# Kernel tuning notes

Measured on AMD Instinct MI355X. Metric: run time of the kernel, lower is better.

The kernel has to match this reference:

```python
import jax, jax.numpy as jnp
import numpy as np

N = 50000
E = 600000
IN_DIM, FEAT_DIM, HID_DIM, OUT_DIM = 256, 128, 128, 64


def _glorot(key, shape):
    fan_in, fan_out = shape[0], shape[1]
    lim = jnp.sqrt(6.0 / (fan_in + fan_out))
    return jax.random.uniform(key, shape, jnp.float32, -lim, lim)


def setup_inputs() -> dict:
    key = jax.random.key(0)
    ks = jax.random.split(key, 10)
    x = jax.random.normal(ks[0], (N, IN_DIM), jnp.float32)
    edge_index = jax.random.randint(ks[1], (2, E), 0, N, jnp.int64)
    return {
        "x": x,
        "edge_index": edge_index,
        # linear_pre: input_dim -> feature_dim
        "W_pre": _glorot(ks[2], (IN_DIM, FEAT_DIM)),
        "b_pre": jnp.zeros((FEAT_DIM,), jnp.float32),
        # conv_first (SAGEConv feature_dim -> hidden_dim): lin_l (neighbors, bias), lin_r (root, no bias)
        "Wl1": _glorot(ks[3], (FEAT_DIM, HID_DIM)),
        "bl1": jnp.zeros((HID_DIM,), jnp.float32),
        "Wr1": _glorot(ks[4], (FEAT_DIM, HID_DIM)),
        # conv_out (SAGEConv hidden_dim -> output_dim)
        "Wl2": _glorot(ks[5], (HID_DIM, OUT_DIM)),
        "bl2": jnp.zeros((OUT_DIM,), jnp.float32),
        "Wr2": _glorot(ks[6], (HID_DIM, OUT_DIM)),
    }


def _sage_conv(x, src, dst, deg_inv, Wl, bl, Wr):
    # mean aggregation of source features at destination nodes
    msgs = x[src]                                            # [E, d]
    aggr = jax.ops.segment_sum(msgs, dst, num_segments=N)    # [N, d]
    aggr = aggr * deg_inv[:, None]
    return aggr @ Wl + bl + x @ Wr


def reference(x, edge_index, W_pre, b_pre, Wl1, bl1, Wr1, Wl2, bl2, Wr2):
    src, dst = edge_index[0], edge_index[1]
    deg = jax.ops.segment_sum(jnp.ones((E,), jnp.float32), dst, num_segments=N)
    deg_inv = jnp.where(deg > 0, 1.0 / jnp.maximum(deg, 1.0), 0.0)

    h = x @ W_pre + b_pre                                    # linear_pre
    h = _sage_conv(h, src, dst, deg_inv, Wl1, bl1, Wr1)      # conv_first
    h = jax.nn.relu(h)
    # dropout: identity in eval mode
    h = _sage_conv(h, src, dst, deg_inv, Wl2, bl2, Wr2)      # conv_out
    norm = jnp.linalg.norm(h, axis=-1, keepdims=True)
    return h / jnp.maximum(norm, 1e-12)                      # F.normalize p=2
```

## Files before the change

### kernel.cpp

```cpp
#include <hip/hip_runtime.h>


#define NN   50000
#define EE   600000
#define NBLK 49
#define NRG  1563
#define GEMM_BLOCKS 512

typedef __attribute__((ext_vector_type(8))) _Float16 h8v;
typedef __attribute__((ext_vector_type(4))) _Float16 h4v;
typedef __attribute__((ext_vector_type(2))) _Float16 h2v;
typedef __attribute__((ext_vector_type(8))) short short8v;
typedef __attribute__((ext_vector_type(4))) float f32x4;

__device__ inline h8v h8zero() {
    return __builtin_bit_cast(h8v, (short8v){0,0,0,0,0,0,0,0});
}

__device__ inline h8v cvt8(const float* __restrict__ p) {
    float4 f0 = *(const float4*)p;
    float4 f1 = *(const float4*)(p + 4);
    h8v a;
    a[0] = (_Float16)f0.x; a[1] = (_Float16)f0.y;
    a[2] = (_Float16)f0.z; a[3] = (_Float16)f0.w;
    a[4] = (_Float16)f1.x; a[5] = (_Float16)f1.y;
    a[6] = (_Float16)f1.z; a[7] = (_Float16)f1.w;
    return a;
}


__global__ __launch_bounds__(256) void k_count(const int* __restrict__ ei,
                                               int* __restrict__ counts) {
    int e = blockIdx.x * 256 + threadIdx.x;
    if (e < EE) atomicAdd(&counts[ei[EE + e]], 1);
}

__global__ __launch_bounds__(256) void k_scan_a(const int* __restrict__ counts,
                                                int* __restrict__ bsums) {
    int b = blockIdx.x, t = threadIdx.x;
    int idx = b * 1024 + t * 4;
    int s = 0;
#pragma unroll
    for (int j = 0; j < 4; ++j)
        if (idx + j < NN) s += counts[idx + j];
#pragma unroll
    for (int off = 32; off > 0; off >>= 1) s += __shfl_down(s, off);
    __shared__ int ls[4];
    if ((t & 63) == 0) ls[t >> 6] = s;
    __syncthreads();
    if (t == 0) bsums[b] = ls[0] + ls[1] + ls[2] + ls[3];
}

__global__ void k_scan_b(int* __restrict__ bsums) {
    int t = threadIdx.x;
    int v = (t < NBLK) ? bsums[t] : 0;
    int orig = v;
#pragma unroll
    for (int off = 1; off < 64; off <<= 1) {
        int u = __shfl_up(v, off);
        if (t >= off) v += u;
    }
    if (t < NBLK) bsums[t] = v - orig;
}

__global__ __launch_bounds__(256) void k_scan_c(const int* __restrict__ counts,
                                                const int* __restrict__ bsums,
                                                int* __restrict__ rowp) {
    int b = blockIdx.x, t = threadIdx.x;
    int lane = t & 63, wave = t >> 6;
    int idx = b * 1024 + t * 4;
    int c[4], s = 0;
#pragma unroll
    for (int j = 0; j < 4; ++j) {
        c[j] = (idx + j < NN) ? counts[idx + j] : 0;
        s += c[j];
    }
    int sv = s;
#pragma unroll
    for (int off = 1; off < 64; off <<= 1) {
        int u = __shfl_up(sv, off);
        if (lane >= off) sv += u;
    }
    __shared__ int lsum[4];
    if (lane == 63) lsum[wave] = sv;
    __syncthreads();
    int woff = 0;
    for (int wv = 0; wv < wave; ++wv) woff += lsum[wv];
    int base = bsums[b] + woff + (sv - s);
#pragma unroll
    for (int j = 0; j < 4; ++j) {
        if (idx + j < NN) { rowp[idx + j] = base; base += c[j]; }
    }
}

__global__ __launch_bounds__(256) void k_scatter(const int* __restrict__ ei,
                                                 const int* __restrict__ rowp,
                                                 int* __restrict__ cursor,
                                                 int* __restrict__ col) {
    int e = blockIdx.x * 256 + threadIdx.x;
    if (e < EE) {
        int d = ei[EE + e];
        int p = atomicAdd(&cursor[d], 1);
        col[rowp[d] + p] = ei[e];
    }
}


__global__ __launch_bounds__(256) void k_fuse(const float* __restrict__ Wpre,
                                              const float* __restrict__ bpre,
                                              const float* __restrict__ Wl1,
                                              const float* __restrict__ Wr1,
                                              _Float16* __restrict__ WAH,
                                              _Float16* __restrict__ WAL,
                                              _Float16* __restrict__ WBH,
                                              _Float16* __restrict__ WBL,
                                              float* __restrict__ bA,
                                              float* __restrict__ bB) {
    int idx = blockIdx.x * 256 + threadIdx.x;
    int which = idx / (257 * 128);
    int rem = idx - which * 257 * 128;
    int i = rem >> 7, j = rem & 127;
    const float* W = which ? Wr1 : Wl1;
    float s = 0.f;
    if (i < 256) {
#pragma unroll 4
        for (int k = 0; k < 128; ++k) s += Wpre[i * 128 + k] * W[k * 128 + j];
        _Float16 h = (_Float16)s;
        _Float16 l = (_Float16)(s - (float)h);
        if (which) { WBH[j * 256 + i] = h; WBL[j * 256 + i] = l; }
        else       { WAH[j * 256 + i] = h; WAL[j * 256 + i] = l; }
    } else {
#pragma unroll 4
        for (int k = 0; k < 128; ++k) s += bpre[k] * W[k * 128 + j];
        if (which) bB[j] = s; else bA[j] = s;
    }
}


__global__ __launch_bounds__(256) void k_pack2(const float* __restrict__ Wl2,
                                               const float* __restrict__ Wr2,
                                               _Float16* __restrict__ W2lH,
                                               _Float16* __restrict__ W2lL,
                                               _Float16* __restrict__ W2rH,
                                               _Float16* __restrict__ W2rL) {
    int idx = blockIdx.x * 256 + threadIdx.x;
    int which = idx >> 13;
    int rem = idx & 8191;
    int k = rem >> 6, m = rem & 63;
    float w = (which ? Wr2 : Wl2)[rem];
    _Float16 h = (_Float16)w;
    _Float16 l = (_Float16)(w - (float)h);
    if (which) { W2rH[m * 128 + k] = h; W2rL[m * 128 + k] = l; }
    else       { W2lH[m * 128 + k] = h; W2lL[m * 128 + k] = l; }
}


__global__ __launch_bounds__(256, 2) void k_gemm_fused(
        const float* __restrict__ x,
        const _Float16* __restrict__ WAH, const _Float16* __restrict__ WAL,
        const _Float16* __restrict__ WBH, const _Float16* __restrict__ WBL,
        const float* __restrict__ bA, const float* __restrict__ bB,
        _Float16* __restrict__ t1, _Float16* __restrict__ r1) {
    const int wave = threadIdx.x >> 6, lane = threadIdx.x & 63;
    const int r = lane & 15, kb = lane >> 4;
    const int gw = blockIdx.x * 4 + wave;
    const int col = ((gw & 7) << 4) + r;

    h8v wah[8], wal[8], wbh[8], wbl[8];
#pragma unroll
    for (int k = 0; k < 8; ++k) {
        size_t off = (size_t)col * 256 + k * 32 + kb * 8;
        wah[k] = *(const h8v*)&WAH[off];
        wal[k] = *(const h8v*)&WAL[off];
        wbh[k] = *(const h8v*)&WBH[off];
        wbl[k] = *(const h8v*)&WBL[off];
    }
    const float biasA = bA[col], biasB = bB[col];

    for (int rg = gw >> 3; rg < NRG; rg += (GEMM_BLOCKS * 4) / 8) {
        const int row0 = rg << 5;
        f32x4 accT[2], accR[2];
#pragma unroll
        for (int a = 0; a < 2; ++a) {
            accT[a] = (f32x4){0.f, 0.f, 0.f, 0.f};
            accR[a] = (f32x4){0.f, 0.f, 0.f, 0.f};
        }
#pragma unroll
        for (int k = 0; k < 8; ++k) {
#pragma unroll
            for (int rt = 0; rt < 2; ++rt) {
                int rr = row0 + rt * 16;
                h8v a = (rr < NN)
                    ? cvt8(&x[(size_t)(rr + r) * 256 + k * 32 + kb * 8])
                    : h8zero();
                accT[rt] = __builtin_amdgcn_mfma_f32_16x16x32_f16(a, wah[k], accT[rt], 0, 0, 0);
                accT[rt] = __builtin_amdgcn_mfma_f32_16x16x32_f16(a, wal[k], accT[rt], 0, 0, 0);
                accR[rt] = __builtin_amdgcn_mfma_f32_16x16x32_f16(a, wbh[k], accR[rt], 0, 0, 0);
                accR[rt] = __builtin_amdgcn_mfma_f32_16x16x32_f16(a, wbl[k], accR[rt], 0, 0, 0);
            }
        }
#pragma unroll
        for (int rt = 0; rt < 2; ++rt) {
            if (row0 + rt * 16 >= NN) continue;
            int rbase = row0 + rt * 16 + kb * 4;
#pragma unroll
            for (int j = 0; j < 4; ++j) {
                t1[(size_t)(rbase + j) * 128 + col] = (_Float16)(accT[rt][j] + biasA);
                r1[(size_t)(rbase + j) * 128 + col] = (_Float16)(accR[rt][j] + biasB);
            }
        }
    }
}


template <int M>
__global__ __launch_bounds__(256, 2) void k_gemm_dual(
        const _Float16* __restrict__ A,
        const _Float16* __restrict__ W1H, const _Float16* __restrict__ W1L,
        const _Float16* __restrict__ W2H, const _Float16* __restrict__ W2L,
        _Float16* __restrict__ T, _Float16* __restrict__ R) {
    constexpr int CS = M / 32;
    const int wave = threadIdx.x >> 6, lane = threadIdx.x & 63;
    const int r = lane & 15, kb = lane >> 4;
    const int gw = blockIdx.x * 4 + wave;
    const int col0 = (gw % CS) << 5;

    h8v b1h[2][4], b1l[2][4], b2h[2][4], b2l[2][4];
#pragma unroll
    for (int nt = 0; nt < 2; ++nt)
#pragma unroll
        for (int k = 0; k < 4; ++k) {
            size_t off = (size_t)(col0 + nt * 16 + r) * 128 + k * 32 + kb * 8;
            b1h[nt][k] = *(const h8v*)&W1H[off];
            b1l[nt][k] = *(const h8v*)&W1L[off];
            b2h[nt][k] = *(const h8v*)&W2H[off];
            b2l[nt][k] = *(const h8v*)&W2L[off];
        }

    const int stride = (GEMM_BLOCKS * 4) / CS;
    for (int rg = gw / CS; rg < NRG; rg += stride) {
        const int row0 = rg << 5;
        f32x4 accT[2][2], accR[2][2];
#pragma unroll
        for (int a = 0; a < 2; ++a)
#pragma unroll
            for (int b = 0; b < 2; ++b) {
                accT[a][b] = (f32x4){0.f, 0.f, 0.f, 0.f};
                accR[a][b] = (f32x4){0.f, 0.f, 0.f, 0.f};
            }
#pragma unroll
        for (int k = 0; k < 4; ++k) {
            h8v ah[2];
#pragma unroll
            for (int rt = 0; rt < 2; ++rt) {
                int rr = row0 + rt * 16;
                ah[rt] = (rr < NN) ? *(const h8v*)&A[(size_t)(rr + r) * 128 + k * 32 + kb * 8]
                                   : h8zero();
            }
#pragma unroll
            for (int rt = 0; rt < 2; ++rt)
#pragma unroll
                for (int nt = 0; nt < 2; ++nt) {
                    accT[rt][nt] = __builtin_amdgcn_mfma_f32_16x16x32_f16(ah[rt], b1h[nt][k], accT[rt][nt], 0, 0, 0);
                    accT[rt][nt] = __builtin_amdgcn_mfma_f32_16x16x32_f16(ah[rt], b1l[nt][k], accT[rt][nt], 0, 0, 0);
                    accR[rt][nt] = __builtin_amdgcn_mfma_f32_16x16x32_f16(ah[rt], b2h[nt][k], accR[rt][nt], 0, 0, 0);
                    accR[rt][nt] = __builtin_amdgcn_mfma_f32_16x16x32_f16(ah[rt], b2l[nt][k], accR[rt][nt], 0, 0, 0);
                }
        }
#pragma unroll
        for (int rt = 0; rt < 2; ++rt) {
            if (row0 + rt * 16 >= NN) continue;
            int rbase = row0 + rt * 16 + kb * 4;
#pragma unroll
            for (int nt = 0; nt < 2; ++nt) {
                int c = col0 + nt * 16 + r;
#pragma unroll
                for (int j = 0; j < 4; ++j) {
                    T[(size_t)(rbase + j) * M + c] = (_Float16)accT[rt][nt][j];
                    R[(size_t)(rbase + j) * M + c] = (_Float16)accR[rt][nt][j];
                }
            }
        }
    }
}


__global__ __launch_bounds__(256) void k_aggr1(const _Float16* __restrict__ t1,
                                               const _Float16* __restrict__ r1,
                                               const int* __restrict__ rowp,
                                               const int* __restrict__ counts,
                                               const int* __restrict__ col,
                                               const float* __restrict__ bl1,
                                               _Float16* __restrict__ h1) {
    int node = blockIdx.x * 4 + (threadIdx.x >> 6);
    int lane = threadIdx.x & 63;
    if (node >= NN) return;
    int half = lane >> 5, sl = lane & 31;
    int e0 = rowp[node], cnt = counts[node];
    float a0 = 0.f, a1 = 0.f, a2 = 0.f, a3 = 0.f;
    const h4v* T = (const h4v*)t1;
    for (int base = 0; base < cnt; base += 64) {
        int m = cnt - base; if (m > 64) m = 64;
        int myS = (base + lane < cnt) ? col[e0 + base + lane] : 0;
        int i = 0;
        for (; i + 8 <= m; i += 8) {
            int s0 = __shfl(myS, i + 0 + half), s1 = __shfl(myS, i + 2 + half);
            int s2 = __shfl(myS, i + 4 + half), s3 = __shfl(myS, i + 6 + half);
            h4v v0 = T[(size_t)s0 * 32 + sl], v1 = T[(size_t)s1 * 32 + sl];
            h4v v2 = T[(size_t)s2 * 32 + sl], v3 = T[(size_t)s3 * 32 + sl];
            a0 += (float)v0[0] + (float)v1[0] + (float)v2[0] + (float)v3[0];
            a1 += (float)v0[1] + (float)v1[1] + (float)v2[1] + (float)v3[1];
            a2 += (float)v0[2] + (float)v1[2] + (float)v2[2] + (float)v3[2];
            a3 += (float)v0[3] + (float)v1[3] + (float)v2[3] + (float)v3[3];
        }
        for (; i < m; i += 2) {
            if (i + half < m) {
                int s = __shfl(myS, i + half);
                h4v v = T[(size_t)s * 32 + sl];
                a0 += (float)v[0]; a1 += (float)v[1];
                a2 += (float)v[2]; a3 += (float)v[3];
            }
        }
    }
    a0 += __shfl_xor(a0, 32); a1 += __shfl_xor(a1, 32);
    a2 += __shfl_xor(a2, 32); a3 += __shfl_xor(a3, 32);
    float di = (cnt > 0) ? 1.0f / (float)cnt : 0.0f;
    h4v rr = ((const h4v*)r1)[(size_t)node * 32 + sl];
    float4 bb = ((const float4*)bl1)[sl];
    if (half == 0) {
        h4v h;
        h[0] = (_Float16)fmaxf(fmaf(a0, di, bb.x + (float)rr[0]), 0.0f);
        h[1] = (_Float16)fmaxf(fmaf(a1, di, bb.y + (float)rr[1]), 0.0f);
        h[2] = (_Float16)fmaxf(fmaf(a2, di, bb.z + (float)rr[2]), 0.0f);
        h[3] = (_Float16)fmaxf(fmaf(a3, di, bb.w + (float)rr[3]), 0.0f);
        ((h4v*)h1)[(size_t)node * 32 + sl] = h;
    }
}


__global__ __launch_bounds__(256) void k_aggr2(const _Float16* __restrict__ t2,
                                               const _Float16* __restrict__ r2,
                                               const int* __restrict__ rowp,
                                               const int* __restrict__ counts,
                                               const int* __restrict__ col,
                                               const float* __restrict__ bl2,
                                               float* __restrict__ out) {
    int node = blockIdx.x * 4 + (threadIdx.x >> 6);
    int lane = threadIdx.x & 63;
    if (node >= NN) return;
    int half = lane >> 5, sl = lane & 31;
    int e0 = rowp[node], cnt = counts[node];
    float ax = 0.f, ay = 0.f;
    const h2v* T = (const h2v*)t2;
    for (int base = 0; base < cnt; base += 64) {
        int m = cnt - base; if (m > 64) m = 64;
        int myS = (base + lane < cnt) ? col[e0 + base + lane] : 0;
        int i = 0;
        for (; i + 8 <= m; i += 8) {
            int s0 = __shfl(myS, i + 0 + half), s1 = __shfl(myS, i + 2 + half);
            int s2 = __shfl(myS, i + 4 + half), s3 = __shfl(myS, i + 6 + half);
            h2v v0 = T[(size_t)s0 * 32 + sl], v1 = T[(size_t)s1 * 32 + sl];
            h2v v2 = T[(size_t)s2 * 32 + sl], v3 = T[(size_t)s3 * 32 + sl];
            ax += (float)v0[0] + (float)v1[0] + (float)v2[0] + (float)v3[0];
            ay += (float)v0[1] + (float)v1[1] + (float)v2[1] + (float)v3[1];
        }
        for (; i < m; i += 2) {
            if (i + half < m) {
                int s = __shfl(myS, i + half);
                h2v v = T[(size_t)s * 32 + sl];
                ax += (float)v[0]; ay += (float)v[1];
            }
        }
    }
    ax += __shfl_xor(ax, 32);
    ay += __shfl_xor(ay, 32);
    float di = (cnt > 0) ? 1.0f / (float)cnt : 0.0f;
    h2v rr = ((const h2v*)r2)[(size_t)node * 32 + sl];
    float2 bb = ((const float2*)bl2)[sl];
    float v0 = fmaf(ax, di, bb.x + (float)rr[0]);
    float v1 = fmaf(ay, di, bb.y + (float)rr[1]);
    float ss = v0 * v0 + v1 * v1;
#pragma unroll
    for (int off = 16; off > 0; off >>= 1) ss += __shfl_xor(ss, off);
    float inv = 1.0f / fmaxf(sqrtf(ss), 1e-12f);
    if (half == 0)
        ((float2*)out)[(size_t)node * 32 + sl] = make_float2(v0 * inv, v1 * inv);
}


extern "C" void kernel_launch(void* const* d_in, const int* in_sizes, int n_in,
                              void* d_out, int out_size, void* d_ws, size_t ws_size,
                              hipStream_t stream) {
    const float* x    = (const float*)d_in[0];
    const int*   ei   = (const int*)d_in[1];
    const float* Wpre = (const float*)d_in[2];
    const float* bpre = (const float*)d_in[3];
    const float* Wl1  = (const float*)d_in[4];
    const float* bl1  = (const float*)d_in[5];
    const float* Wr1  = (const float*)d_in[6];
    const float* Wl2  = (const float*)d_in[7];
    const float* bl2  = (const float*)d_in[8];
    const float* Wr2  = (const float*)d_in[9];
    float* out = (float*)d_out;

    char* w = (char*)d_ws;
    int* counts = (int*)w;  w += (size_t)NN * 4;
    int* cursor = (int*)w;  w += (size_t)NN * 4;
    int* rowp   = (int*)w;  w += (size_t)NN * 4;
    int* bsums  = (int*)w;  w += 256;
    int* col    = (int*)w;  w += (size_t)EE * 4;
    _Float16* WAH  = (_Float16*)w; w += (size_t)256 * 128 * 2;
    _Float16* WAL  = (_Float16*)w; w += (size_t)256 * 128 * 2;
    _Float16* WBH  = (_Float16*)w; w += (size_t)256 * 128 * 2;
    _Float16* WBL  = (_Float16*)w; w += (size_t)256 * 128 * 2;
    float*    bA   = (float*)w;    w += 128 * 4;
    float*    bB   = (float*)w;    w += 128 * 4;
    _Float16* W2lH = (_Float16*)w; w += (size_t)128 * 64 * 2;
    _Float16* W2lL = (_Float16*)w; w += (size_t)128 * 64 * 2;
    _Float16* W2rH = (_Float16*)w; w += (size_t)128 * 64 * 2;
    _Float16* W2rL = (_Float16*)w; w += (size_t)128 * 64 * 2;
    _Float16* t1   = (_Float16*)w; w += (size_t)NN * 128 * 2;
    _Float16* r1   = (_Float16*)w; w += (size_t)NN * 128 * 2;
    _Float16* h1   = (_Float16*)w; w += (size_t)NN * 128 * 2;
    _Float16* t2   = (_Float16*)w; w += (size_t)NN * 64 * 2;
    _Float16* r2   = (_Float16*)w; w += (size_t)NN * 64 * 2;

    hipMemsetAsync(counts, 0, (size_t)NN * 8, stream);

    dim3 b256(256);
    dim3 gE((EE + 255) / 256);
    k_count<<<gE, b256, 0, stream>>>(ei, counts);
    k_scan_a<<<dim3(NBLK), b256, 0, stream>>>(counts, bsums);
    k_scan_b<<<dim3(1), dim3(64), 0, stream>>>(bsums);
    k_scan_c<<<dim3(NBLK), b256, 0, stream>>>(counts, bsums, rowp);
    k_scatter<<<gE, b256, 0, stream>>>(ei, rowp, cursor, col);

    k_fuse<<<dim3(257), b256, 0, stream>>>(Wpre, bpre, Wl1, Wr1,
                                           WAH, WAL, WBH, WBL, bA, bB);
    k_pack2<<<dim3(64), b256, 0, stream>>>(Wl2, Wr2, W2lH, W2lL, W2rH, W2rL);

    dim3 gP(GEMM_BLOCKS);
    k_gemm_fused<<<gP, b256, 0, stream>>>(x, WAH, WAL, WBH, WBL, bA, bB, t1, r1);
    k_aggr1<<<dim3((NN + 3) / 4), b256, 0, stream>>>(t1, r1, rowp, counts, col, bl1, h1);
    k_gemm_dual<64><<<gP, b256, 0, stream>>>(h1, W2lH, W2lL, W2rH, W2rL, t2, r2);
    k_aggr2<<<dim3((NN + 3) / 4), b256, 0, stream>>>(t2, r2, rowp, counts, col, bl2, out);
}
```

Measured before the change: 322.2 us.

## Pre-convert x to fp16 and retile GEMMs so each wave owns one output matrix

Adds a separate kernel that converts x to fp16 once. Both GEMM kernels are restructured so each wave computes one 16-column slice of a single output (T or R) over 64-row groups, instead of both outputs over 32-row groups. The weight fusion and layer-2 packing kernels are merged into one launch. This roughly halves per-wave weight register use and the repeated float-to-half conversion work. In exchange it adds an extra 25.6 MB fp16 copy of x written and reread, and each A tile is now loaded by twice as many waves.

```diff
diff --git a/kernel.cpp b/kernel.cpp
--- a/kernel.cpp
+++ b/kernel.cpp
@@ -4,7 +4,7 @@
 #define NN   50000
 #define EE   600000
 #define NBLK 49
-#define NRG  1563
+#define NRG64 782
 #define GEMM_BLOCKS 512
 
 typedef __attribute__((ext_vector_type(8))) _Float16 h8v;
@@ -15,17 +15,6 @@
 
 __device__ inline h8v h8zero() {
     return __builtin_bit_cast(h8v, (short8v){0,0,0,0,0,0,0,0});
-}
-
-__device__ inline h8v cvt8(const float* __restrict__ p) {
-    float4 f0 = *(const float4*)p;
-    float4 f1 = *(const float4*)(p + 4);
-    h8v a;
-    a[0] = (_Float16)f0.x; a[1] = (_Float16)f0.y;
-    a[2] = (_Float16)f0.z; a[3] = (_Float16)f0.w;
-    a[4] = (_Float16)f1.x; a[5] = (_Float16)f1.y;
-    a[6] = (_Float16)f1.z; a[7] = (_Float16)f1.w;
-    return a;
 }
 
 
@@ -106,180 +95,178 @@
 }
 
 
-__global__ __launch_bounds__(256) void k_fuse(const float* __restrict__ Wpre,
+__global__ __launch_bounds__(256) void k_cvt(const float* __restrict__ in,
+                                             _Float16* __restrict__ outp, int n4) {
+    int i = blockIdx.x * 256 + threadIdx.x;
+    if (i >= n4) return;
+    float4 v = ((const float4*)in)[i];
+    h4v o;
+    o[0] = (_Float16)v.x; o[1] = (_Float16)v.y;
+    o[2] = (_Float16)v.z; o[3] = (_Float16)v.w;
+    ((h4v*)outp)[i] = o;
+}
+
+
+__global__ __launch_bounds__(256) void k_prep(const float* __restrict__ Wpre,
                                               const float* __restrict__ bpre,
                                               const float* __restrict__ Wl1,
                                               const float* __restrict__ Wr1,
+                                              const float* __restrict__ Wl2,
+                                              const float* __restrict__ Wr2,
                                               _Float16* __restrict__ WAH,
                                               _Float16* __restrict__ WAL,
                                               _Float16* __restrict__ WBH,
                                               _Float16* __restrict__ WBL,
                                               float* __restrict__ bA,
-                                              float* __restrict__ bB) {
+                                              float* __restrict__ bB,
+                                              _Float16* __restrict__ W2lH,
+                                              _Float16* __restrict__ W2lL,
+                                              _Float16* __restrict__ W2rH,
+                                              _Float16* __restrict__ W2rL) {
     int idx = blockIdx.x * 256 + threadIdx.x;
-    int which = idx / (257 * 128);
-    int rem = idx - which * 257 * 128;
-    int i = rem >> 7, j = rem & 127;
-    const float* W = which ? Wr1 : Wl1;
-    float s = 0.f;
-    if (i < 256) {
+    if (idx < 65792) {
+        int which = idx / (257 * 128);
+        int rem = idx - which * 257 * 128;
+        int i = rem >> 7, j = rem & 127;
+        const float* W = which ? Wr1 : Wl1;
+        float s = 0.f;
+        if (i < 256) {
 #pragma unroll 4
-        for (int k = 0; k < 128; ++k) s += Wpre[i * 128 + k] * W[k * 128 + j];
-        _Float16 h = (_Float16)s;
-        _Float16 l = (_Float16)(s - (float)h);
-        if (which) { WBH[j * 256 + i] = h; WBL[j * 256 + i] = l; }
-        else       { WAH[j * 256 + i] = h; WAL[j * 256 + i] = l; }
+            for (int k = 0; k < 128; ++k) s += Wpre[i * 128 + k] * W[k * 128 + j];
+            _Float16 h = (_Float16)s;
+            _Float16 l = (_Float16)(s - (float)h);
+            if (which) { WBH[j * 256 + i] = h; WBL[j * 256 + i] = l; }
+            else       { WAH[j * 256 + i] = h; WAL[j * 256 + i] = l; }
+        } else {
+#pragma unroll 4
+            for (int k = 0; k < 128; ++k) s += bpre[k] * W[k * 128 + j];
+            if (which) bB[j] = s; else bA[j] = s;
+        }
     } else {
-#pragma unroll 4
-        for (int k = 0; k < 128; ++k) s += bpre[k] * W[k * 128 + j];
-        if (which) bB[j] = s; else bA[j] = s;
-    }
-}
-
-
-__global__ __launch_bounds__(256) void k_pack2(const float* __restrict__ Wl2,
-                                               const float* __restrict__ Wr2,
-                                               _Float16* __restrict__ W2lH,
-                                               _Float16* __restrict__ W2lL,
-                                               _Float16* __restrict__ W2rH,
-                                               _Float16* __restrict__ W2rL) {
-    int idx = blockIdx.x * 256 + threadIdx.x;
-    int which = idx >> 13;
-    int rem = idx & 8191;
-    int k = rem >> 6, m = rem & 63;
-    float w = (which ? Wr2 : Wl2)[rem];
-    _Float16 h = (_Float16)w;
-    _Float16 l = (_Float16)(w - (float)h);
-    if (which) { W2rH[m * 128 + k] = h; W2rL[m * 128 + k] = l; }
-    else       { W2lH[m * 128 + k] = h; W2lL[m * 128 + k] = l; }
+        int idx2 = idx - 65792;
+        int which = idx2 >> 13;
+        int rem = idx2 & 8191;
+        int k = rem >> 6, m = rem & 63;
+        float w = (which ? Wr2 : Wl2)[rem];
+        _Float16 h = (_Float16)w;
+        _Float16 l = (_Float16)(w - (float)h);
+        if (which) { W2rH[m * 128 + k] = h; W2rL[m * 128 + k] = l; }
+        else       { W2lH[m * 128 + k] = h; W2lL[m * 128 + k] = l; }
+    }
 }
 
 
 __global__ __launch_bounds__(256, 2) void k_gemm_fused(
-        const float* __restrict__ x,
+        const _Float16* __restrict__ xh,
         const _Float16* __restrict__ WAH, const _Float16* __restrict__ WAL,
         const _Float16* __restrict__ WBH, const _Float16* __restrict__ WBL,
         const float* __restrict__ bA, const float* __restrict__ bB,
         _Float16* __restrict__ t1, _Float16* __restrict__ r1) {
     const int wave = threadIdx.x >> 6, lane = threadIdx.x & 63;
     const int r = lane & 15, kb = lane >> 4;
-    const int gw = blockIdx.x * 4 + wave;
-    const int col = ((gw & 7) << 4) + r;
-
-    h8v wah[8], wal[8], wbh[8], wbl[8];
+    const int s = ((blockIdx.x & 3) << 2) + wave;
+    const int sel = s >> 3;
+    const int col = ((s & 7) << 4) + r;
+    const _Float16* __restrict__ WH = sel ? WBH : WAH;
+    const _Float16* __restrict__ WL = sel ? WBL : WAL;
+    _Float16* __restrict__ dst = sel ? r1 : t1;
+    const float bias = (sel ? bB : bA)[col];
+
+    h8v wh[8], wl[8];
 #pragma unroll
     for (int k = 0; k < 8; ++k) {
         size_t off = (size_t)col * 256 + k * 32 + kb * 8;
-        wah[k] = *(const h8v*)&WAH[off];
-        wal[k] = *(const h8v*)&WAL[off];
-        wbh[k] = *(const h8v*)&WBH[off];
-        wbl[k] = *(const h8v*)&WBL[off];
-    }
-    const float biasA = bA[col], biasB = bB[col];
-
-    for (int rg = gw >> 3; rg < NRG; rg += (GEMM_BLOCKS * 4) / 8) {
-        const int row0 = rg << 5;
-        f32x4 accT[2], accR[2];
-#pragma unroll
-        for (int a = 0; a < 2; ++a) {
-            accT[a] = (f32x4){0.f, 0.f, 0.f, 0.f};
-            accR[a] = (f32x4){0.f, 0.f, 0.f, 0.f};
-        }
+        wh[k] = *(const h8v*)&WH[off];
+        wl[k] = *(const h8v*)&WL[off];
+    }
+
+    for (int rg = blockIdx.x >> 2; rg < NRG64; rg += GEMM_BLOCKS / 4) {
+        const int row0 = rg << 6;
+        f32x4 acc[4];
+#pragma unroll
+        for (int a = 0; a < 4; ++a) acc[a] = (f32x4){0.f, 0.f, 0.f, 0.f};
+
 #pragma unroll
         for (int k = 0; k < 8; ++k) {
-#pragma unroll
-            for (int rt = 0; rt < 2; ++rt) {
+            h8v a[4];
+#pragma unroll
+            for (int rt = 0; rt < 4; ++rt) {
                 int rr = row0 + rt * 16;
-                h8v a = (rr < NN)
-                    ? cvt8(&x[(size_t)(rr + r) * 256 + k * 32 + kb * 8])
+                a[rt] = (rr < NN)
+                    ? *(const h8v*)&xh[(size_t)(rr + r) * 256 + k * 32 + kb * 8]
                     : h8zero();
-                accT[rt] = __builtin_amdgcn_mfma_f32_16x16x32_f16(a, wah[k], accT[rt], 0, 0, 0);
-                accT[rt] = __builtin_amdgcn_mfma_f32_16x16x32_f16(a, wal[k], accT[rt], 0, 0, 0);
-                accR[rt] = __builtin_amdgcn_mfma_f32_16x16x32_f16(a, wbh[k], accR[rt], 0, 0, 0);
-                accR[rt] = __builtin_amdgcn_mfma_f32_16x16x32_f16(a, wbl[k], accR[rt], 0, 0, 0);
-            }
-        }
-#pragma unroll
-        for (int rt = 0; rt < 2; ++rt) {
-            if (row0 + rt * 16 >= NN) continue;
-            int rbase = row0 + rt * 16 + kb * 4;
-#pragma unroll
-            for (int j = 0; j < 4; ++j) {
-                t1[(size_t)(rbase + j) * 128 + col] = (_Float16)(accT[rt][j] + biasA);
-                r1[(size_t)(rbase + j) * 128 + col] = (_Float16)(accR[rt][j] + biasB);
-            }
-        }
-    }
-}
-
-
-template <int M>
-__global__ __launch_bounds__(256, 2) void k_gemm_dual(
+            }
+#pragma unroll
+            for (int rt = 0; rt < 4; ++rt) {
+                acc[rt] = __builtin_amdgcn_mfma_f32_16x16x32_f16(a[rt], wh[k], acc[rt], 0, 0, 0);
+                acc[rt] = __builtin_amdgcn_mfma_f32_16x16x32_f16(a[rt], wl[k], acc[rt], 0, 0, 0);
+            }
+        }
+#pragma unroll
+        for (int rt = 0; rt < 4; ++rt) {
+            int rr = row0 + rt * 16;
+            if (rr >= NN) continue;
+            int rbase = rr + kb * 4;
+#pragma unroll
+            for (int j = 0; j < 4; ++j)
+                dst[(size_t)(rbase + j) * 128 + col] = (_Float16)(acc[rt][j] + bias);
+        }
+    }
+}
+
+
+__global__ __launch_bounds__(256, 2) void k_gemm_dual2(
         const _Float16* __restrict__ A,
         const _Float16* __restrict__ W1H, const _Float16* __restrict__ W1L,
         const _Float16* __restrict__ W2H, const _Float16* __restrict__ W2L,
         _Float16* __restrict__ T, _Float16* __restrict__ R) {
-    constexpr int CS = M / 32;
     const int wave = threadIdx.x >> 6, lane = threadIdx.x & 63;
     const int r = lane & 15, kb = lane >> 4;
-    const int gw = blockIdx.x * 4 + wave;
-    const int col0 = (gw % CS) << 5;
-
-    h8v b1h[2][4], b1l[2][4], b2h[2][4], b2l[2][4];
-#pragma unroll
-    for (int nt = 0; nt < 2; ++nt)
+    const int s = ((blockIdx.x & 1) << 2) + wave;
+    const int sel = s >> 2;
+    const int col = ((s & 3) << 4) + r;
+    const _Float16* __restrict__ WH = sel ? W2H : W1H;
+    const _Float16* __restrict__ WL = sel ? W2L : W1L;
+    _Float16* __restrict__ dst = sel ? R : T;
+
+    h8v wh[4], wl[4];
+#pragma unroll
+    for (int k = 0; k < 4; ++k) {
+        size_t off = (size_t)col * 128 + k * 32 + kb * 8;
+        wh[k] = *(const h8v*)&WH[off];
+        wl[k] = *(const h8v*)&WL[off];
+    }
+
+    for (int rg = blockIdx.x >> 1; rg < NRG64; rg += GEMM_BLOCKS / 2) {
+        const int row0 = rg << 6;
+        f32x4 acc[4];
+#pragma unroll
+        for (int a = 0; a < 4; ++a) acc[a] = (f32x4){0.f, 0.f, 0.f, 0.f};
+
 #pragma unroll
         for (int k = 0; k < 4; ++k) {
-            size_t off = (size_t)(col0 + nt * 16 + r) * 128 + k * 32 + kb * 8;
-            b1h[nt][k] = *(const h8v*)&W1H[off];
-            b1l[nt][k] = *(const h8v*)&W1L[off];
-            b2h[nt][k] = *(const h8v*)&W2H[off];
-            b2l[nt][k] = *(const h8v*)&W2L[off];
-        }
-
-    const int stride = (GEMM_BLOCKS * 4) / CS;
-    for (int rg = gw / CS; rg < NRG; rg += stride) {
-        const int row0 = rg << 5;
-        f32x4 accT[2][2], accR[2][2];
-#pragma unroll
-        for (int a = 0; a < 2; ++a)
-#pragma unroll
-            for (int b = 0; b < 2; ++b) {
-                accT[a][b] = (f32x4){0.f, 0.f, 0.f, 0.f};
-                accR[a][b] = (f32x4){0.f, 0.f, 0.f, 0.f};
-            }
-#pragma unroll
-        for (int k = 0; k < 4; ++k) {
-            h8v ah[2];
-#pragma unroll
-            for (int rt = 0; rt < 2; ++rt) {
+            h8v a[4];
+#pragma unroll
+            for (int rt = 0; rt < 4; ++rt) {
                 int rr = row0 + rt * 16;
-                ah[rt] = (rr < NN) ? *(const h8v*)&A[(size_t)(rr + r) * 128 + k * 32 + kb * 8]
-                                   : h8zero();
-            }
-#pragma unroll
-            for (int rt = 0; rt < 2; ++rt)
-#pragma unroll
-                for (int nt = 0; nt < 2; ++nt) {
-                    accT[rt][nt] = __builtin_amdgcn_mfma_f32_16x16x32_f16(ah[rt], b1h[nt][k], accT[rt][nt], 0, 0, 0);
-                    accT[rt][nt] = __builtin_amdgcn_mfma_f32_16x16x32_f16(ah[rt], b1l[nt][k], accT[rt][nt], 0, 0, 0);
-                    accR[rt][nt] = __builtin_amdgcn_mfma_f32_16x16x32_f16(ah[rt], b2h[nt][k], accR[rt][nt], 0, 0, 0);
-                    accR[rt][nt] = __builtin_amdgcn_mfma_f32_16x16x32_f16(ah[rt], b2l[nt][k], accR[rt][nt], 0, 0, 0);
-                }
-        }
-#pragma unroll
-        for (int rt = 0; rt < 2; ++rt) {
-            if (row0 + rt * 16 >= NN) continue;
-            int rbase = row0 + rt * 16 + kb * 4;
-#pragma unroll
-            for (int nt = 0; nt < 2; ++nt) {
-                int c = col0 + nt * 16 + r;
-#pragma unroll
-                for (int j = 0; j < 4; ++j) {
-                    T[(size_t)(rbase + j) * M + c] = (_Float16)accT[rt][nt][j];
-                    R[(size_t)(rbase + j) * M + c] = (_Float16)accR[rt][nt][j];
-                }
-            }
+                a[rt] = (rr < NN)
+                    ? *(const h8v*)&A[(size_t)(rr + r) * 128 + k * 32 + kb * 8]
+                    : h8zero();
+            }
+#pragma unroll
+            for (int rt = 0; rt < 4; ++rt) {
+                acc[rt] = __builtin_amdgcn_mfma_f32_16x16x32_f16(a[rt], wh[k], acc[rt], 0, 0, 0);
+                acc[rt] = __builtin_amdgcn_mfma_f32_16x16x32_f16(a[rt], wl[k], acc[rt], 0, 0, 0);
+            }
+        }
+#pragma unroll
+        for (int rt = 0; rt < 4; ++rt) {
+            int rr = row0 + rt * 16;
+            if (rr >= NN) continue;
+            int rbase = rr + kb * 4;
+#pragma unroll
+            for (int j = 0; j < 4; ++j)
+                dst[(size_t)(rbase + j) * 64 + col] = (_Float16)acc[rt][j];
         }
     }
 }
@@ -419,6 +406,7 @@
     _Float16* W2lL = (_Float16*)w; w += (size_t)128 * 64 * 2;
     _Float16* W2rH = (_Float16*)w; w += (size_t)128 * 64 * 2;
     _Float16* W2rL = (_Float16*)w; w += (size_t)128 * 64 * 2;
+    _Float16* xh   = (_Float16*)w; w += (size_t)NN * 256 * 2;
     _Float16* t1   = (_Float16*)w; w += (size_t)NN * 128 * 2;
     _Float16* r1   = (_Float16*)w; w += (size_t)NN * 128 * 2;
     _Float16* h1   = (_Float16*)w; w += (size_t)NN * 128 * 2;
@@ -435,13 +423,14 @@
     k_scan_c<<<dim3(NBLK), b256, 0, stream>>>(counts, bsums, rowp);
     k_scatter<<<gE, b256, 0, stream>>>(ei, rowp, cursor, col);
 
-    k_fuse<<<dim3(257), b256, 0, stream>>>(Wpre, bpre, Wl1, Wr1,
-                                           WAH, WAL, WBH, WBL, bA, bB);
-    k_pack2<<<dim3(64), b256, 0, stream>>>(Wl2, Wr2, W2lH, W2lL, W2rH, W2rL);
+    k_cvt<<<dim3(NN * 256 / 4 / 256), b256, 0, stream>>>(x, xh, NN * 256 / 4);
+    k_prep<<<dim3(321), b256, 0, stream>>>(Wpre, bpre, Wl1, Wr1, Wl2, Wr2,
+                                           WAH, WAL, WBH, WBL, bA, bB,
+                                           W2lH, W2lL, W2rH, W2rL);
 
     dim3 gP(GEMM_BLOCKS);
-    k_gemm_fused<<<gP, b256, 0, stream>>>(x, WAH, WAL, WBH, WBL, bA, bB, t1, r1);
+    k_gemm_fused<<<gP, b256, 0, stream>>>(xh, WAH, WAL, WBH, WBL, bA, bB, t1, r1);
     k_aggr1<<<dim3((NN + 3) / 4), b256, 0, stream>>>(t1, r1, rowp, counts, col, bl1, h1);
-    k_gemm_dual<64><<<gP, b256, 0, stream>>>(h1, W2lH, W2lL, W2rH, W2rL, t2, r2);
+    k_gemm_dual2<<<gP, b256, 0, stream>>>(h1, W2lH, W2lL, W2rH, W2rL, t2, r2);
     k_aggr2<<<dim3((NN + 3) / 4), b256, 0, stream>>>(t2, r2, rowp, counts, col, bl2, out);
 }
```

New measurement: 317.1 us. About the same (-1.6%).
